# Performance work log

Hardware: AMD Instinct MI355X
Metric: run time of the kernel (lower is better)

Reference implementation:

```python
import jax, jax.numpy as jnp
import numpy as np

HEAD_SIZE = 64


def setup_inputs() -> dict:
    key = jax.random.key(0)
    ks = jax.random.split(key, 4)
    B, S, H, D = 8, 4096, 768, HEAD_SIZE
    scale = 1.0 / np.sqrt(H)
    return {
        "x": jax.random.normal(ks[0], (B, S, H), dtype=jnp.float32),
        "Wq": jax.random.normal(ks[1], (H, D), dtype=jnp.float32) * scale,
        "bq": jnp.zeros((D,), dtype=jnp.float32),
        "Wk": jax.random.normal(ks[2], (H, D), dtype=jnp.float32) * scale,
        "bk": jnp.zeros((D,), dtype=jnp.float32),
        "Wv": jax.random.normal(ks[3], (H, D), dtype=jnp.float32) * scale,
        "bv": jnp.zeros((D,), dtype=jnp.float32),
    }


def reference(x, Wq, bq, Wk, bk, Wv, bv):
    # x: [B, S, H]
    B, S, H = x.shape
    D = Wq.shape[1]
    q = x @ Wq + bq  # [B, S, D]
    k = x @ Wk + bk
    v = x @ Wv + bv
    # naive full score matrix [B, S, S]
    scores = jnp.einsum("bsd,btd->bst", q, k)
    causal = jnp.tril(jnp.ones((S, S), dtype=bool))  # lower-triangular mask
    scores = jnp.where(causal[None, :, :], scores, -jnp.inf)
    attn = jax.nn.softmax(scores / jnp.sqrt(jnp.float32(D)), axis=-1)
    # dropout is identity in eval/deterministic reference
    out = jnp.einsum("bst,btd->bsd", attn, v)  # [B, S, D]
    return out
```

## Files before the change

### kernel.cpp

```cpp
#include <hip/hip_runtime.h>

typedef unsigned short u16;
typedef __bf16 bf16_t;
typedef bf16_t bf16x8 __attribute__((ext_vector_type(8)));
typedef float f32x4 __attribute__((ext_vector_type(4)));
typedef u16 u16x8 __attribute__((ext_vector_type(8)));

#define B_ 8
#define S_ 4096
#define H_ 768
#define M_ (B_ * S_)

__device__ __forceinline__ u16 f2b(float f) {
  unsigned u = __float_as_uint(f);
  u += 0x7fffu + ((u >> 16) & 1u);
  return (u16)(u >> 16);
}

__device__ __forceinline__ void gl_lds16(const void* g, void* l) {
  __builtin_amdgcn_global_load_lds(
      (const __attribute__((address_space(1))) void*)g,
      (__attribute__((address_space(3))) void*)l, 16, 0, 0);
}

__global__ __launch_bounds__(256) void wconv_k(const float* __restrict__ Wq,
                                               const float* __restrict__ Wk,
                                               const float* __restrict__ Wv,
                                               u16* __restrict__ WbT) {
  __shared__ float wt[64 * 68];
  const int tid = threadIdx.x;
  int mat = blockIdx.x / 12;
  int k0 = (blockIdx.x % 12) * 64;
  const float* W = (mat == 0) ? Wq : ((mat == 1) ? Wk : Wv);
  int r = tid >> 2, c0 = (tid & 3) * 16;
  const float* src = W + (size_t)(k0 + r) * 64 + c0;
#pragma unroll
  for (int j = 0; j < 16; j += 4)
    *(float4*)&wt[r * 68 + c0 + j] = *(const float4*)(src + j);
  __syncthreads();
  int d = tid >> 2;
  u16* dst = WbT + (size_t)(mat * 64 + d) * 768 + k0 + c0;
  u16x8 o0, o1;
#pragma unroll
  for (int j = 0; j < 8; ++j) o0[j] = f2b(wt[(c0 + j) * 68 + d]);
#pragma unroll
  for (int j = 0; j < 8; ++j) o1[j] = f2b(wt[(c0 + 8 + j) * 68 + d]);
  *(u16x8*)dst = o0;
  *(u16x8*)(dst + 8) = o1;
}

__global__ __launch_bounds__(256) void qkv_k(const float* __restrict__ x,
                                             const u16* __restrict__ WbT,
                                             const float* __restrict__ bq,
                                             const float* __restrict__ bk,
                                             const float* __restrict__ bv,
                                             u16* __restrict__ qb,
                                             u16* __restrict__ kb,
                                             u16* __restrict__ vbT) {
  __shared__ __align__(16) u16 smem[2 * 2560 + 2 * 7680];
  const int tid = threadIdx.x;
  const int w = tid >> 6, ln = tid & 15, qd = (tid >> 4) & 3;
  const int row0 = blockIdx.x * 64;

  const f32x4 z4 = {0.f, 0.f, 0.f, 0.f};
  f32x4 acc[4][3];
#pragma unroll
  for (int rt = 0; rt < 4; ++rt)
#pragma unroll
    for (int ct = 0; ct < 3; ++ct) acc[rt][ct] = z4;

  const int xr = tid >> 2, xc = (tid & 3) * 8;
  float4 xf0, xf1;
  u16x8 wf[3];

  auto load_t = [&](int kt) {
    const float* sx = x + (size_t)(row0 + xr) * 768 + kt * 32 + xc;
    xf0 = *(const float4*)sx;
    xf1 = *(const float4*)(sx + 4);
#pragma unroll
    for (int i = 0; i < 3; ++i) {
      int c = i * 256 + tid;
      int r = c >> 2, off = (c & 3) * 8;
      wf[i] = *(const u16x8*)(WbT + (size_t)r * 768 + kt * 32 + off);
    }
  };

  load_t(0);
  for (int kt = 0; kt < 24; ++kt) {
    u16* xs = smem + (kt & 1) * 2560;
    u16* wsb = smem + 5120 + (kt & 1) * 7680;
    {
      u16x8 v;
      v[0] = f2b(xf0.x); v[1] = f2b(xf0.y); v[2] = f2b(xf0.z); v[3] = f2b(xf0.w);
      v[4] = f2b(xf1.x); v[5] = f2b(xf1.y); v[6] = f2b(xf1.z); v[7] = f2b(xf1.w);
      *(u16x8*)&xs[xr * 40 + xc] = v;
#pragma unroll
      for (int i = 0; i < 3; ++i) {
        int c = i * 256 + tid;
        int r = c >> 2, off = (c & 3) * 8;
        *(u16x8*)&wsb[r * 40 + off] = wf[i];
      }
    }
    if (kt < 23) load_t(kt + 1);
    __syncthreads();
    bf16x8 af[4], bfr[3];
#pragma unroll
    for (int rt = 0; rt < 4; ++rt)
      af[rt] = *(const bf16x8*)&xs[(rt * 16 + ln) * 40 + qd * 8];
#pragma unroll
    for (int ct = 0; ct < 3; ++ct)
      bfr[ct] = *(const bf16x8*)&wsb[(w * 48 + ct * 16 + ln) * 40 + qd * 8];
#pragma unroll
    for (int rt = 0; rt < 4; ++rt)
#pragma unroll
      for (int ct = 0; ct < 3; ++ct)
        acc[rt][ct] = __builtin_amdgcn_mfma_f32_16x16x32_bf16(
            af[rt], bfr[ct], acc[rt][ct], 0, 0, 0);
    __syncthreads();
  }

  u16* vt = smem;
#pragma unroll
  for (int ct = 0; ct < 3; ++ct) {
    int col = w * 48 + ct * 16 + ln;
    int mat = col >> 6, d = col & 63;
    if (mat < 2) {
      const float* bp = (mat == 0) ? bq : bk;
      u16* op = (mat == 0) ? qb : kb;
      float bias = bp[d];
      float scale = (mat == 0) ? 0.18033688011112042f : 1.0f;
#pragma unroll
      for (int rt = 0; rt < 4; ++rt)
#pragma unroll
        for (int r = 0; r < 4; ++r)
          op[(size_t)(row0 + rt * 16 + qd * 4 + r) * 64 + d] =
              f2b((acc[rt][ct][r] + bias) * scale);
    } else {
      float bias = bv[d];
#pragma unroll
      for (int rt = 0; rt < 4; ++rt)
#pragma unroll
        for (int r = 0; r < 4; ++r)
          vt[d * 72 + rt * 16 + qd * 4 + r] = f2b(acc[rt][ct][r] + bias);
    }
  }
  __syncthreads();
  {
    int d = tid >> 2, so = (tid & 3) * 16;
    int b = row0 >> 12, s0 = row0 & 4095;
    u16* dst = vbT + ((size_t)b * 64 + d) * 4096 + s0 + so;
    *(u16x8*)dst = *(const u16x8*)&vt[d * 72 + so];
    *(u16x8*)(dst + 8) = *(const u16x8*)&vt[d * 72 + so + 8];
  }
}

__global__ __launch_bounds__(256) void attn_k(const u16* __restrict__ qb,
                                              const u16* __restrict__ kb,
                                              const u16* __restrict__ vbT,
                                              float* __restrict__ po0,
                                              float* __restrict__ po1,
                                              float* __restrict__ pl0,
                                              float* __restrict__ pl1) {
  __shared__ __align__(16) u16 ks[2][4096];
  __shared__ __align__(16) u16 vs[2][4096];
  __shared__ __align__(16) u16 ps[4 * 16 * 88];
  const int tid = threadIdx.x;
  const int w = tid >> 6, ln = tid & 15, qd = (tid >> 4) & 3;
  const int id = blockIdx.x;
  int b, qi, tstart, tcount;
  if (id < 256) {
    b = id & 7; qi = 32 + (id >> 3); tstart = 0; tcount = 32;
  } else if (id < 512) {
    b = id & 7; qi = 63 - ((id - 256) >> 3); tstart = 32; tcount = qi - 31;
  } else {
    b = id & 7; qi = 31 - ((id - 512) >> 3); tstart = 0; tcount = qi + 1;
  }
  const int q0 = qi * 64, q0w = q0 + w * 16;
  const int base = b * S_;
  const u16* kg = kb + (size_t)base * 64;
  const u16* vg = vbT + (size_t)b * 64 * 4096;

  bf16x8 qf[2];
  {
    const u16* qrow = qb + (size_t)(base + q0w + ln) * 64;
    qf[0] = *(const bf16x8*)(qrow + qd * 8);
    qf[1] = *(const bf16x8*)(qrow + 32 + qd * 8);
  }
  const f32x4 z4 = {0.f, 0.f, 0.f, 0.f};
  f32x4 o[4] = {z4, z4, z4, z4};
  float lp[4] = {0.f, 0.f, 0.f, 0.f};
  u16* psw = ps + w * (16 * 88);
  const int lr = (tid & 63) >> 3, csl = tid & 7;

  auto prefetch = [&](int bufi, int tile) {
    const u16* kt_ = kg + (size_t)tile * 4096;
    const u16* vt_ = vg + tile * 64;
#pragma unroll
    for (int i = 0; i < 2; ++i) {
      int r0 = w * 16 + i * 8;
      int r = r0 + lr;
      int c = csl ^ (r & 7);
      gl_lds16(kt_ + r * 64 + c * 8, &ks[bufi][r0 * 64]);
      gl_lds16(vt_ + (size_t)r * 4096 + c * 8, &vs[bufi][r0 * 64]);
    }
  };

  prefetch(0, tstart);
  int buf = 0;
  for (int it = 0; it < tcount; ++it) {
    __syncthreads();
    if (it + 1 < tcount) prefetch(buf ^ 1, tstart + it + 1);
    const int t0a = (tstart + it) * 64;

    f32x4 s[4] = {z4, z4, z4, z4};
#pragma unroll
    for (int kc = 0; kc < 2; ++kc) {
      int cs = (kc * 4 + qd) ^ (ln & 7);
#pragma unroll
      for (int nt = 0; nt < 4; ++nt) {
        bf16x8 bfr = *(const bf16x8*)&ks[buf][(nt * 16 + ln) * 64 + cs * 8];
        s[nt] = __builtin_amdgcn_mfma_f32_16x16x32_bf16(qf[kc], bfr, s[nt], 0, 0, 0);
      }
    }
    if (t0a == q0) {
#pragma unroll
      for (int nt = 0; nt < 4; ++nt) {
        int tg = t0a + nt * 16 + ln;
#pragma unroll
        for (int r = 0; r < 4; ++r)
          if (tg > q0w + qd * 4 + r) s[nt][r] = -INFINITY;
      }
    }
#pragma unroll
    for (int nt = 0; nt < 4; ++nt)
#pragma unroll
      for (int r = 0; r < 4; ++r) {
        float p = __builtin_amdgcn_exp2f(s[nt][r]);
        lp[r] += p;
        psw[(qd * 4 + r) * 88 + nt * 16 + ln] = f2b(p);
      }
#pragma unroll
    for (int kc = 0; kc < 2; ++kc) {
      bf16x8 afr = *(const bf16x8*)&psw[ln * 88 + kc * 32 + qd * 8];
      int cs = (kc * 4 + qd) ^ (ln & 7);
#pragma unroll
      for (int nt = 0; nt < 4; ++nt) {
        bf16x8 bfr = *(const bf16x8*)&vs[buf][(nt * 16 + ln) * 64 + cs * 8];
        o[nt] = __builtin_amdgcn_mfma_f32_16x16x32_bf16(afr, bfr, o[nt], 0, 0, 0);
      }
    }
    buf ^= 1;
  }

#pragma unroll
  for (int r = 0; r < 4; ++r) {
    float v = lp[r];
    v += __shfl_xor(v, 1); v += __shfl_xor(v, 2);
    v += __shfl_xor(v, 4); v += __shfl_xor(v, 8);
    lp[r] = v;
  }
  float* op = (tstart == 0) ? po0 : po1;
  float* lpt = (tstart == 0) ? pl0 : pl1;
#pragma unroll
  for (int r = 0; r < 4; ++r) {
    int row = base + q0w + qd * 4 + r;
#pragma unroll
    for (int nt = 0; nt < 4; ++nt)
      op[(size_t)row * 64 + nt * 16 + ln] = o[nt][r];
    if (ln == 0) lpt[row] = lp[r];
  }
}

__global__ __launch_bounds__(256) void comb_k(const float* __restrict__ po0,
                                              const float* __restrict__ po1,
                                              const float* __restrict__ pl0,
                                              const float* __restrict__ pl1,
                                              float* __restrict__ out) {
  int idx = blockIdx.x * 256 + threadIdx.x;
  int r = idx >> 4, d0 = (idx & 15) * 4;
  int qi = (r & 4095) >> 6;
  float4 a = *(const float4*)(po0 + (size_t)r * 64 + d0);
  float l = pl0[r];
  if (qi >= 32) {
    float4 c = *(const float4*)(po1 + (size_t)r * 64 + d0);
    a.x += c.x; a.y += c.y; a.z += c.z; a.w += c.w;
    l += pl1[r];
  }
  float inv = 1.0f / l;
  a.x *= inv; a.y *= inv; a.z *= inv; a.w *= inv;
  *(float4*)(out + (size_t)r * 64 + d0) = a;
}

extern "C" void kernel_launch(void* const* d_in, const int* in_sizes, int n_in,
                              void* d_out, int out_size, void* d_ws, size_t ws_size,
                              hipStream_t stream) {
  const float* x  = (const float*)d_in[0];
  const float* Wq = (const float*)d_in[1];
  const float* bq = (const float*)d_in[2];
  const float* Wk = (const float*)d_in[3];
  const float* bk = (const float*)d_in[4];
  const float* Wv = (const float*)d_in[5];
  const float* bv = (const float*)d_in[6];
  float* out = (float*)d_out;

  char* wsp = (char*)d_ws;
  u16* WbT = (u16*)wsp;
  u16* qb  = (u16*)(wsp + 294912);
  u16* kb  = (u16*)(wsp + 4489216);
  u16* vbT = (u16*)(wsp + 8683520);
  float* po0 = (float*)(wsp + 12877824);
  float* po1 = (float*)(wsp + 21266432);
  float* pl0 = (float*)(wsp + 29655040);
  float* pl1 = (float*)(wsp + 29786112);

  hipLaunchKernelGGL(wconv_k, dim3(36), dim3(256), 0, stream, Wq, Wk, Wv, WbT);
  hipLaunchKernelGGL(qkv_k, dim3(512), dim3(256), 0, stream,
                     x, WbT, bq, bk, bv, qb, kb, vbT);
  hipLaunchKernelGGL(attn_k, dim3(768), dim3(256), 0, stream,
                     qb, kb, vbT, po0, po1, pl0, pl1);
  hipLaunchKernelGGL(comb_k, dim3(2048), dim3(256), 0, stream,
                     po0, po1, pl0, pl1, out);
}
```

Measured before the change: 225.8 us.

## Rework attention to 128-row query tiles with chunked split-K and direct global K/V loads

```diff
diff --git a/kernel.cpp b/kernel.cpp
--- a/kernel.cpp
+++ b/kernel.cpp
@@ -15,12 +15,6 @@
   unsigned u = __float_as_uint(f);
   u += 0x7fffu + ((u >> 16) & 1u);
   return (u16)(u >> 16);
-}
-
-__device__ __forceinline__ void gl_lds16(const void* g, void* l) {
-  __builtin_amdgcn_global_load_lds(
-      (const __attribute__((address_space(1))) void*)g,
-      (__attribute__((address_space(3))) void*)l, 16, 0, 0);
 }
 
 __global__ __launch_bounds__(256) void wconv_k(const float* __restrict__ Wq,
@@ -84,25 +78,32 @@
       wf[i] = *(const u16x8*)(WbT + (size_t)r * 768 + kt * 32 + off);
     }
   };
-
-  load_t(0);
-  for (int kt = 0; kt < 24; ++kt) {
+  auto write_b = [&](int kt) {
     u16* xs = smem + (kt & 1) * 2560;
     u16* wsb = smem + 5120 + (kt & 1) * 7680;
-    {
-      u16x8 v;
-      v[0] = f2b(xf0.x); v[1] = f2b(xf0.y); v[2] = f2b(xf0.z); v[3] = f2b(xf0.w);
-      v[4] = f2b(xf1.x); v[5] = f2b(xf1.y); v[6] = f2b(xf1.z); v[7] = f2b(xf1.w);
-      *(u16x8*)&xs[xr * 40 + xc] = v;
-#pragma unroll
-      for (int i = 0; i < 3; ++i) {
-        int c = i * 256 + tid;
-        int r = c >> 2, off = (c & 3) * 8;
-        *(u16x8*)&wsb[r * 40 + off] = wf[i];
-      }
-    }
-    if (kt < 23) load_t(kt + 1);
+    u16x8 v;
+    v[0] = f2b(xf0.x); v[1] = f2b(xf0.y); v[2] = f2b(xf0.z); v[3] = f2b(xf0.w);
+    v[4] = f2b(xf1.x); v[5] = f2b(xf1.y); v[6] = f2b(xf1.z); v[7] = f2b(xf1.w);
+    *(u16x8*)&xs[xr * 40 + xc] = v;
+#pragma unroll
+    for (int i = 0; i < 3; ++i) {
+      int c = i * 256 + tid;
+      int r = c >> 2, off = (c & 3) * 8;
+      *(u16x8*)&wsb[r * 40 + off] = wf[i];
+    }
+  };
+
+  load_t(0);
+  write_b(0);
+  load_t(1);
+  for (int kt = 0; kt < 24; ++kt) {
     __syncthreads();
+    if (kt < 23) {
+      write_b(kt + 1);
+      if (kt < 22) load_t(kt + 2);
+    }
+    u16* xs = smem + (kt & 1) * 2560;
+    u16* wsb = smem + 5120 + (kt & 1) * 7680;
     bf16x8 af[4], bfr[3];
 #pragma unroll
     for (int rt = 0; rt < 4; ++rt)
@@ -154,137 +155,125 @@
   }
 }
 
-__global__ __launch_bounds__(256) void attn_k(const u16* __restrict__ qb,
-                                              const u16* __restrict__ kb,
-                                              const u16* __restrict__ vbT,
-                                              float* __restrict__ po0,
-                                              float* __restrict__ po1,
-                                              float* __restrict__ pl0,
-                                              float* __restrict__ pl1) {
-  __shared__ __align__(16) u16 ks[2][4096];
-  __shared__ __align__(16) u16 vs[2][4096];
+__global__ __launch_bounds__(256, 3) void attn_k(const u16* __restrict__ qb,
+                                                 const u16* __restrict__ kb,
+                                                 const u16* __restrict__ vbT,
+                                                 float* __restrict__ po,
+                                                 float* __restrict__ pl) {
   __shared__ __align__(16) u16 ps[4 * 16 * 88];
   const int tid = threadIdx.x;
   const int w = tid >> 6, ln = tid & 15, qd = (tid >> 4) & 3;
   const int id = blockIdx.x;
-  int b, qi, tstart, tcount;
-  if (id < 256) {
-    b = id & 7; qi = 32 + (id >> 3); tstart = 0; tcount = 32;
-  } else if (id < 512) {
-    b = id & 7; qi = 63 - ((id - 256) >> 3); tstart = 32; tcount = qi - 31;
-  } else {
-    b = id & 7; qi = 31 - ((id - 512) >> 3); tstart = 0; tcount = qi + 1;
-  }
-  const int q0 = qi * 64, q0w = q0 + w * 16;
+  const int b = id & 7;
+  int t = id >> 3;
+  int qi = 31, rem = t;
+  for (;;) {
+    int c = (2 * qi + 2 + 15) >> 4;
+    if (rem < c) break;
+    rem -= c;
+    --qi;
+  }
+  const int chunk = rem;
+  const int tstart = rem * 16;
+  int tcount = 2 * qi + 2 - tstart;
+  if (tcount > 16) tcount = 16;
+  const int q0 = qi * 128;
+  const int q0w = q0 + w * 32;
   const int base = b * S_;
   const u16* kg = kb + (size_t)base * 64;
   const u16* vg = vbT + (size_t)b * 64 * 4096;
 
-  bf16x8 qf[2];
-  {
-    const u16* qrow = qb + (size_t)(base + q0w + ln) * 64;
-    qf[0] = *(const bf16x8*)(qrow + qd * 8);
-    qf[1] = *(const bf16x8*)(qrow + 32 + qd * 8);
+  bf16x8 qf[2][2];
+#pragma unroll
+  for (int qt = 0; qt < 2; ++qt) {
+    const u16* qrow = qb + (size_t)(base + q0w + qt * 16 + ln) * 64;
+    qf[qt][0] = *(const bf16x8*)(qrow + qd * 8);
+    qf[qt][1] = *(const bf16x8*)(qrow + 32 + qd * 8);
   }
   const f32x4 z4 = {0.f, 0.f, 0.f, 0.f};
-  f32x4 o[4] = {z4, z4, z4, z4};
-  float lp[4] = {0.f, 0.f, 0.f, 0.f};
+  f32x4 o[2][4] = {{z4, z4, z4, z4}, {z4, z4, z4, z4}};
+  float lp[2][4] = {{0.f, 0.f, 0.f, 0.f}, {0.f, 0.f, 0.f, 0.f}};
   u16* psw = ps + w * (16 * 88);
-  const int lr = (tid & 63) >> 3, csl = tid & 7;
-
-  auto prefetch = [&](int bufi, int tile) {
-    const u16* kt_ = kg + (size_t)tile * 4096;
-    const u16* vt_ = vg + tile * 64;
-#pragma unroll
-    for (int i = 0; i < 2; ++i) {
-      int r0 = w * 16 + i * 8;
-      int r = r0 + lr;
-      int c = csl ^ (r & 7);
-      gl_lds16(kt_ + r * 64 + c * 8, &ks[bufi][r0 * 64]);
-      gl_lds16(vt_ + (size_t)r * 4096 + c * 8, &vs[bufi][r0 * 64]);
-    }
-  };
-
-  prefetch(0, tstart);
-  int buf = 0;
+
   for (int it = 0; it < tcount; ++it) {
-    __syncthreads();
-    if (it + 1 < tcount) prefetch(buf ^ 1, tstart + it + 1);
     const int t0a = (tstart + it) * 64;
-
-    f32x4 s[4] = {z4, z4, z4, z4};
-#pragma unroll
-    for (int kc = 0; kc < 2; ++kc) {
-      int cs = (kc * 4 + qd) ^ (ln & 7);
+    bf16x8 kf[2][4], vf[2][4];
+#pragma unroll
+    for (int kc = 0; kc < 2; ++kc)
 #pragma unroll
       for (int nt = 0; nt < 4; ++nt) {
-        bf16x8 bfr = *(const bf16x8*)&ks[buf][(nt * 16 + ln) * 64 + cs * 8];
-        s[nt] = __builtin_amdgcn_mfma_f32_16x16x32_bf16(qf[kc], bfr, s[nt], 0, 0, 0);
+        kf[kc][nt] = *(const bf16x8*)(kg + (size_t)(t0a + nt * 16 + ln) * 64 +
+                                      kc * 32 + qd * 8);
+        vf[kc][nt] = *(const bf16x8*)(vg + (size_t)(nt * 16 + ln) * 4096 + t0a +
+                                      kc * 32 + qd * 8);
       }
-    }
-    if (t0a == q0) {
-#pragma unroll
-      for (int nt = 0; nt < 4; ++nt) {
-        int tg = t0a + nt * 16 + ln;
-#pragma unroll
-        for (int r = 0; r < 4; ++r)
-          if (tg > q0w + qd * 4 + r) s[nt][r] = -INFINITY;
+#pragma unroll
+    for (int qt = 0; qt < 2; ++qt) {
+      f32x4 s[4] = {z4, z4, z4, z4};
+#pragma unroll
+      for (int kc = 0; kc < 2; ++kc)
+#pragma unroll
+        for (int nt = 0; nt < 4; ++nt)
+          s[nt] = __builtin_amdgcn_mfma_f32_16x16x32_bf16(qf[qt][kc], kf[kc][nt],
+                                                          s[nt], 0, 0, 0);
+      if (t0a >= q0) {
+#pragma unroll
+        for (int nt = 0; nt < 4; ++nt) {
+          int tg = t0a + nt * 16 + ln;
+#pragma unroll
+          for (int r = 0; r < 4; ++r)
+            if (tg > q0w + qt * 16 + qd * 4 + r) s[nt][r] = -INFINITY;
+        }
       }
-    }
-#pragma unroll
-    for (int nt = 0; nt < 4; ++nt)
-#pragma unroll
-      for (int r = 0; r < 4; ++r) {
-        float p = __builtin_amdgcn_exp2f(s[nt][r]);
-        lp[r] += p;
-        psw[(qd * 4 + r) * 88 + nt * 16 + ln] = f2b(p);
+#pragma unroll
+      for (int nt = 0; nt < 4; ++nt)
+#pragma unroll
+        for (int r = 0; r < 4; ++r) {
+          float p = __builtin_amdgcn_exp2f(s[nt][r]);
+          lp[qt][r] += p;
+          psw[(qd * 4 + r) * 88 + nt * 16 + ln] = f2b(p);
+        }
+#pragma unroll
+      for (int kc = 0; kc < 2; ++kc) {
+        bf16x8 afr = *(const bf16x8*)&psw[ln * 88 + kc * 32 + qd * 8];
+#pragma unroll
+        for (int nt = 0; nt < 4; ++nt)
+          o[qt][nt] = __builtin_amdgcn_mfma_f32_16x16x32_bf16(afr, vf[kc][nt],
+                                                              o[qt][nt], 0, 0, 0);
       }
-#pragma unroll
-    for (int kc = 0; kc < 2; ++kc) {
-      bf16x8 afr = *(const bf16x8*)&psw[ln * 88 + kc * 32 + qd * 8];
-      int cs = (kc * 4 + qd) ^ (ln & 7);
-#pragma unroll
-      for (int nt = 0; nt < 4; ++nt) {
-        bf16x8 bfr = *(const bf16x8*)&vs[buf][(nt * 16 + ln) * 64 + cs * 8];
-        o[nt] = __builtin_amdgcn_mfma_f32_16x16x32_bf16(afr, bfr, o[nt], 0, 0, 0);
-      }
-    }
-    buf ^= 1;
-  }
-
-#pragma unroll
-  for (int r = 0; r < 4; ++r) {
-    float v = lp[r];
-    v += __shfl_xor(v, 1); v += __shfl_xor(v, 2);
-    v += __shfl_xor(v, 4); v += __shfl_xor(v, 8);
-    lp[r] = v;
-  }
-  float* op = (tstart == 0) ? po0 : po1;
-  float* lpt = (tstart == 0) ? pl0 : pl1;
-#pragma unroll
-  for (int r = 0; r < 4; ++r) {
-    int row = base + q0w + qd * 4 + r;
-#pragma unroll
-    for (int nt = 0; nt < 4; ++nt)
-      op[(size_t)row * 64 + nt * 16 + ln] = o[nt][r];
-    if (ln == 0) lpt[row] = lp[r];
-  }
-}
-
-__global__ __launch_bounds__(256) void comb_k(const float* __restrict__ po0,
-                                              const float* __restrict__ po1,
-                                              const float* __restrict__ pl0,
-                                              const float* __restrict__ pl1,
+    }
+  }
+
+  float* poc = po + (size_t)chunk * M_ * 64;
+  float* plc = pl + (size_t)chunk * M_;
+#pragma unroll
+  for (int qt = 0; qt < 2; ++qt)
+#pragma unroll
+    for (int r = 0; r < 4; ++r) {
+      float v = lp[qt][r];
+      v += __shfl_xor(v, 1); v += __shfl_xor(v, 2);
+      v += __shfl_xor(v, 4); v += __shfl_xor(v, 8);
+      int row = base + q0w + qt * 16 + qd * 4 + r;
+#pragma unroll
+      for (int nt = 0; nt < 4; ++nt)
+        poc[(size_t)row * 64 + nt * 16 + ln] = o[qt][nt][r];
+      if (ln == 0) plc[row] = v;
+    }
+}
+
+__global__ __launch_bounds__(256) void comb_k(const float* __restrict__ po,
+                                              const float* __restrict__ pl,
                                               float* __restrict__ out) {
   int idx = blockIdx.x * 256 + threadIdx.x;
   int r = idx >> 4, d0 = (idx & 15) * 4;
-  int qi = (r & 4095) >> 6;
-  float4 a = *(const float4*)(po0 + (size_t)r * 64 + d0);
-  float l = pl0[r];
-  if (qi >= 32) {
-    float4 c = *(const float4*)(po1 + (size_t)r * 64 + d0);
-    a.x += c.x; a.y += c.y; a.z += c.z; a.w += c.w;
-    l += pl1[r];
+  int qi = (r & 4095) >> 7;
+  int nch = (2 * qi + 2 + 15) >> 4;
+  float4 a = {0.f, 0.f, 0.f, 0.f};
+  float l = 0.f;
+  for (int c = 0; c < nch; ++c) {
+    float4 p = *(const float4*)(po + (size_t)c * M_ * 64 + (size_t)r * 64 + d0);
+    a.x += p.x; a.y += p.y; a.z += p.z; a.w += p.w;
+    l += pl[(size_t)c * M_ + r];
   }
   float inv = 1.0f / l;
   a.x *= inv; a.y *= inv; a.z *= inv; a.w *= inv;
@@ -304,20 +293,17 @@
   float* out = (float*)d_out;
 
   char* wsp = (char*)d_ws;
-  u16* WbT = (u16*)wsp;
-  u16* qb  = (u16*)(wsp + 294912);
-  u16* kb  = (u16*)(wsp + 4489216);
-  u16* vbT = (u16*)(wsp + 8683520);
-  float* po0 = (float*)(wsp + 12877824);
-  float* po1 = (float*)(wsp + 21266432);
-  float* pl0 = (float*)(wsp + 29655040);
-  float* pl1 = (float*)(wsp + 29786112);
+  u16* WbT  = (u16*)wsp;
+  u16* qb   = (u16*)(wsp + 294912);
+  u16* kb   = (u16*)(wsp + 4489216);
+  u16* vbT  = (u16*)(wsp + 8683520);
+  float* po = (float*)(wsp + 12877824);
+  float* pl = (float*)(wsp + 46432256);
 
   hipLaunchKernelGGL(wconv_k, dim3(36), dim3(256), 0, stream, Wq, Wk, Wv, WbT);
   hipLaunchKernelGGL(qkv_k, dim3(512), dim3(256), 0, stream,
                      x, WbT, bq, bk, bv, qb, kb, vbT);
-  hipLaunchKernelGGL(attn_k, dim3(768), dim3(256), 0, stream,
-                     qb, kb, vbT, po0, po1, pl0, pl1);
-  hipLaunchKernelGGL(comb_k, dim3(2048), dim3(256), 0, stream,
-                     po0, po1, pl0, pl1, out);
-}
+  hipLaunchKernelGGL(attn_k, dim3(640), dim3(256), 0, stream,
+                     qb, kb, vbT, po, pl);
+  hipLaunchKernelGGL(comb_k, dim3(2048), dim3(256), 0, stream, po, pl, out);
+}
```

Measured after the change: 269.1 us. +19.2%, slower.
